# Performance work log

Measured on AMD Instinct MI355X. Metric: run time of the kernel, lower is better.

## Reference

```python
import jax, jax.numpy as jnp
import numpy as np


def _squash_global(v):
    # Faithful to torch: v.norm() with no dim -> global Frobenius norm (scalar).
    n2 = jnp.sum(v * v)
    n = jnp.sqrt(n2)
    scale = n2 / (1.0 + n2)
    return scale * v / n


def setup_inputs() -> dict:
    key = jax.random.key(0)
    k1, k2 = jax.random.split(key)
    B, R, Ci = 128, 1152, 8
    C, O = 10, 16
    x = jax.random.normal(k1, (B, R, Ci), dtype=jnp.float32)
    W = jax.random.normal(k2, (C, R, Ci, O), dtype=jnp.float32)  # routing_weights ~ randn
    return {"x": x, "W": W, "num_iterations": 3}


def reference(x, W, num_iterations):
    # prediction_vectors: [C, B, R, 1, O]
    u = jnp.einsum('bri,crio->cbro', x, W)[:, :, :, None, :]
    logits = jnp.zeros_like(u)
    v = None
    for _ in range(num_iterations):
        # batch_softmax: cat over dim0 + legacy softmax(dim=1 of 4D) == softmax over
        # the num_route_nodes axis (axis 2 here).
        c = jax.nn.softmax(logits, axis=2)
        s = jnp.sum(c * u, axis=2, keepdims=True)  # [C, B, 1, 1, O]
        v = _squash_global(s)
        logits = logits + u * v
    return v
```

## Files before the change

### kernel.cpp

```cpp
#include <hip/hip_runtime.h>
#include <math.h>

#define Bn   128
#define Rn   1152
#define CIn  8
#define Cn   10
#define On   16
#define BO   2048
#define CBO  20480
#define NSEG 18
#define XSTR 132
#define WSTR 132


template<int PASS>
__global__ __launch_bounds__(256, 2)
void pass_kernel(const float* __restrict__ X, const float* __restrict__ Wt,
                 const float* __restrict__ Sprev, const float* __restrict__ N2,
                 float* __restrict__ PT, float* __restrict__ PL)
{
    __shared__ float xs[32 * XSTR];
    __shared__ float wsh[On * WSTR];

    const int blk = blockIdx.x;
    const int c   = blk / 72;
    const int rem = blk - c * 72;
    const int bt  = rem / 18;
    const int seg = rem - bt * 18;
    const int b0  = bt * 32;
    const int rs0 = seg * 64;

    const int tid = threadIdx.x;
    const int rr  = tid & 3;
    const int og  = (tid >> 2) & 3;
    const int bq  = tid >> 4;

    float vs[2][4];
    if (PASS > 1) {
        float coef[PASS];
        #pragma unroll
        for (int t = 0; t < PASS - 1; ++t) {
            const float n2 = N2[t];
            coef[t] = n2 / ((1.0f + n2) * sqrtf(n2)) * 1.4426950408889634f;
        }
        #pragma unroll
        for (int j = 0; j < 2; ++j) {
            const int b = b0 + bq + 16 * j;
            #pragma unroll
            for (int m = 0; m < 4; ++m) {
                const int idx = c * BO + b * On + (og + 4 * m);
                float a = 0.0f;
                #pragma unroll
                for (int t = 0; t < PASS - 1; ++t)
                    a = fmaf(coef[t], Sprev[t * CBO + idx], a);
                vs[j][m] = a;
            }
        }
    }

    float tacc[2][4], lacc[2][4];
    #pragma unroll
    for (int j = 0; j < 2; ++j)
        #pragma unroll
        for (int m = 0; m < 4; ++m) { tacc[j][m] = 0.0f; lacc[j][m] = 0.0f; }

    for (int ch = 0; ch < 4; ++ch) {
        const int r0 = rs0 + ch * 16;

        {
            const float* xbase = X + (size_t)b0 * (Rn * CIn) + (size_t)r0 * CIn;
            #pragma unroll
            for (int l = tid; l < 1024; l += 256) {
                const int bl  = l >> 5;
                const int off = (l & 31) << 2;
                const float4 v = *(const float4*)(xbase + (size_t)bl * (Rn * CIn) + off);
                *(float4*)(xs + bl * XSTR + off) = v;
            }
        }
        {
            const float* wbase = Wt + (size_t)c * (Rn * CIn * On) + (size_t)r0 * (CIn * On);
            #pragma unroll
            for (int l = tid; l < 512; l += 256) {
                const int rl = l >> 5;
                const int i  = (l >> 2) & 7;
                const int o4 = (l & 3) << 2;
                const float4 v = *(const float4*)(wbase + rl * 128 + i * On + o4);
                wsh[(o4 + 0) * WSTR + rl * 8 + i] = v.x;
                wsh[(o4 + 1) * WSTR + rl * 8 + i] = v.y;
                wsh[(o4 + 2) * WSTR + rl * 8 + i] = v.z;
                wsh[(o4 + 3) * WSTR + rl * 8 + i] = v.w;
            }
        }
        __syncthreads();

        #pragma unroll
        for (int k = 0; k < 4; ++k) {
            const int r = (k << 2) | rr;
            float4 xa[2], xb[2];
            #pragma unroll
            for (int j = 0; j < 2; ++j) {
                const float* p = xs + (bq + 16 * j) * XSTR + r * 8;
                xa[j] = *(const float4*)p;
                xb[j] = *(const float4*)(p + 4);
            }
            float4 wa[4], wb[4];
            #pragma unroll
            for (int m = 0; m < 4; ++m) {
                const float* q = wsh + (og + 4 * m) * WSTR + r * 8;
                wa[m] = *(const float4*)q;
                wb[m] = *(const float4*)(q + 4);
            }
            #pragma unroll
            for (int j = 0; j < 2; ++j) {
                #pragma unroll
                for (int m = 0; m < 4; ++m) {
                    float u = xa[j].x * wa[m].x;
                    u = fmaf(xa[j].y, wa[m].y, u);
                    u = fmaf(xa[j].z, wa[m].z, u);
                    u = fmaf(xa[j].w, wa[m].w, u);
                    u = fmaf(xb[j].x, wb[m].x, u);
                    u = fmaf(xb[j].y, wb[m].y, u);
                    u = fmaf(xb[j].z, wb[m].z, u);
                    u = fmaf(xb[j].w, wb[m].w, u);
                    if (PASS == 1) {
                        tacc[j][m] += u;
                    } else {
                        const float e = exp2f(u * vs[j][m]);
                        lacc[j][m] += e;
                        tacc[j][m] = fmaf(e, u, tacc[j][m]);
                    }
                }
            }
        }
        __syncthreads();
    }

    #pragma unroll
    for (int j = 0; j < 2; ++j) {
        const int b = b0 + bq + 16 * j;
        #pragma unroll
        for (int m = 0; m < 4; ++m) {
            float tv = tacc[j][m];
            tv += __shfl_xor(tv, 1);
            tv += __shfl_xor(tv, 2);
            float lv = 0.0f;
            if (PASS > 1) {
                lv = lacc[j][m];
                lv += __shfl_xor(lv, 1);
                lv += __shfl_xor(lv, 2);
            }
            if (rr == 0) {
                const int idx = seg * CBO + c * BO + b * On + (og + 4 * m);
                PT[idx] = tv;
                if (PASS > 1) PL[idx] = lv;
            }
        }
    }
}

template<int PASS>
__global__ __launch_bounds__(256)
void combine_kernel(const float* __restrict__ PT, const float* __restrict__ PL,
                    float* __restrict__ Sout, float* __restrict__ n2out)
{
    const int i = blockIdx.x * 256 + threadIdx.x;
    float T = 0.0f, L = 0.0f;
    #pragma unroll
    for (int s = 0; s < NSEG; ++s) T += PT[s * CBO + i];
    if (PASS == 1) {
        L = (float)Rn;
    } else {
        #pragma unroll
        for (int s = 0; s < NSEG; ++s) L += PL[s * CBO + i];
    }
    const float sv = T / L;
    Sout[i] = sv;
    float sq = sv * sv;
    #pragma unroll
    for (int d = 1; d < 64; d <<= 1) sq += __shfl_xor(sq, d);
    __shared__ float red[4];
    if ((threadIdx.x & 63) == 0) red[threadIdx.x >> 6] = sq;
    __syncthreads();
    if (threadIdx.x == 0)
        atomicAdd(n2out, red[0] + red[1] + red[2] + red[3]);
}

__global__ __launch_bounds__(256)
void final_kernel(const float* __restrict__ S, const float* __restrict__ n2p,
                  float* __restrict__ out)
{
    const int i = blockIdx.x * 256 + threadIdx.x;
    const float n2 = *n2p;
    const float coef = n2 / ((1.0f + n2) * sqrtf(n2));
    out[i] = coef * S[i];
}

extern "C" void kernel_launch(void* const* d_in, const int* in_sizes, int n_in,
                              void* d_out, int out_size, void* d_ws, size_t ws_size,
                              hipStream_t stream)
{
    const float* X  = (const float*)d_in[0];
    const float* Wt = (const float*)d_in[1];
    float* ws = (float*)d_ws;
    float* N2 = ws;
    float* PT = ws + 4;
    float* PL = PT + NSEG * CBO;
    float* S  = PL + NSEG * CBO;

    hipMemsetAsync(ws, 0, 16, stream);

    pass_kernel<1><<<720, 256, 0, stream>>>(X, Wt, S, N2, PT, PL);
    combine_kernel<1><<<80, 256, 0, stream>>>(PT, PL, S + 0 * CBO, N2 + 0);
    pass_kernel<2><<<720, 256, 0, stream>>>(X, Wt, S, N2, PT, PL);
    combine_kernel<2><<<80, 256, 0, stream>>>(PT, PL, S + 1 * CBO, N2 + 1);
    pass_kernel<3><<<720, 256, 0, stream>>>(X, Wt, S, N2, PT, PL);
    combine_kernel<3><<<80, 256, 0, stream>>>(PT, PL, S + 2 * CBO, N2 + 2);
    final_kernel<<<80, 256, 0, stream>>>(S + 2 * CBO, N2 + 2, (float*)d_out);
}
```

Measured before the change: 135.1 us.

## Transpose x once and stream W through scalar loads instead of LDS tiles

Adds a one-time transpose of x into a route-major layout, so each lane (one batch element) loads its x row with coalesced float4 reads. The pass kernel no longer stages tiles in shared memory. Each wave takes a contiguous chunk of 12 routes, and W is read through wave-uniform (readfirstlane) addresses, so the hardware can serve it with scalar loads. Each thread now holds all 16 outputs for one batch element, and partial sums are reduced across the 4 waves through LDS, with fewer segments (24) left for the combine kernel. This removes the per-chunk LDS staging, barriers and transposed W stores, at the cost of an extra transpose kernel and more registers per thread.

```diff
diff --git a/kernel.cpp b/kernel.cpp
--- a/kernel.cpp
+++ b/kernel.cpp
@@ -8,34 +8,40 @@
 #define On   16
 #define BO   2048
 #define CBO  20480
-#define NSEG 18
-#define XSTR 132
-#define WSTR 132
+#define RC   12
+#define NSEG 96
+#define PSEG 24
 
+__global__ __launch_bounds__(256)
+void transpose_x(const float* __restrict__ X, float* __restrict__ XT)
+{
+    const int r = blockIdx.x;
+    const int b = threadIdx.x & 127;
+    const int g = threadIdx.x >> 7;
+    float4 v = *(const float4*)(X + (size_t)b * (Rn * CIn) + r * CIn + g * 4);
+    ((float4*)XT)[r * 256 + g * 128 + b] = v;
+}
 
 template<int PASS>
 __global__ __launch_bounds__(256, 2)
-void pass_kernel(const float* __restrict__ X, const float* __restrict__ Wt,
+void pass_kernel(const float* __restrict__ XT, const float* __restrict__ W,
                  const float* __restrict__ Sprev, const float* __restrict__ N2,
                  float* __restrict__ PT, float* __restrict__ PL)
 {
-    __shared__ float xs[32 * XSTR];
-    __shared__ float wsh[On * WSTR];
+    __shared__ float red[4][64][34];
 
-    const int blk = blockIdx.x;
-    const int c   = blk / 72;
-    const int rem = blk - c * 72;
-    const int bt  = rem / 18;
-    const int seg = rem - bt * 18;
-    const int b0  = bt * 32;
-    const int rs0 = seg * 64;
+    const int blk  = blockIdx.x;
+    const int c    = blk / 48;
+    const int rem  = blk - c * 48;
+    const int bh   = rem / 24;
+    const int segq = rem - bh * 24;
+    const int tid  = threadIdx.x;
+    const int w    = tid >> 6;
+    const int lane = tid & 63;
+    const int b    = bh * 64 + lane;
+    const int r0   = __builtin_amdgcn_readfirstlane((segq * 4 + w) * RC);
 
-    const int tid = threadIdx.x;
-    const int rr  = tid & 3;
-    const int og  = (tid >> 2) & 3;
-    const int bq  = tid >> 4;
-
-    float vs[2][4];
+    float vs[16];
     if (PASS > 1) {
         float coef[PASS];
         #pragma unroll
@@ -43,118 +49,78 @@
             const float n2 = N2[t];
             coef[t] = n2 / ((1.0f + n2) * sqrtf(n2)) * 1.4426950408889634f;
         }
+        const float* sp = Sprev + c * BO + b * On;
         #pragma unroll
-        for (int j = 0; j < 2; ++j) {
-            const int b = b0 + bq + 16 * j;
+        for (int q = 0; q < 4; ++q) {
+            float4 a = make_float4(0.f, 0.f, 0.f, 0.f);
             #pragma unroll
-            for (int m = 0; m < 4; ++m) {
-                const int idx = c * BO + b * On + (og + 4 * m);
-                float a = 0.0f;
-                #pragma unroll
-                for (int t = 0; t < PASS - 1; ++t)
-                    a = fmaf(coef[t], Sprev[t * CBO + idx], a);
-                vs[j][m] = a;
+            for (int t = 0; t < PASS - 1; ++t) {
+                const float4 s4 = *(const float4*)(sp + t * CBO + q * 4);
+                a.x = fmaf(coef[t], s4.x, a.x);
+                a.y = fmaf(coef[t], s4.y, a.y);
+                a.z = fmaf(coef[t], s4.z, a.z);
+                a.w = fmaf(coef[t], s4.w, a.w);
+            }
+            vs[q * 4 + 0] = a.x; vs[q * 4 + 1] = a.y;
+            vs[q * 4 + 2] = a.z; vs[q * 4 + 3] = a.w;
+        }
+    }
+
+    float tacc[16], lacc[16];
+    #pragma unroll
+    for (int o = 0; o < 16; ++o) { tacc[o] = 0.0f; lacc[o] = 0.0f; }
+
+    const float4* XT4 = (const float4*)XT;
+    for (int rr = 0; rr < RC; ++rr) {
+        const int r = r0 + rr;
+        const float4 xa = XT4[r * 256 + b];
+        const float4 xb = XT4[r * 256 + 128 + b];
+        const int woff = __builtin_amdgcn_readfirstlane((c * Rn + r) * 128);
+        const float* wr = W + woff;
+        #pragma unroll
+        for (int o = 0; o < 16; ++o) {
+            float u = xa.x * wr[o];
+            u = fmaf(xa.y, wr[16 + o], u);
+            u = fmaf(xa.z, wr[32 + o], u);
+            u = fmaf(xa.w, wr[48 + o], u);
+            u = fmaf(xb.x, wr[64 + o], u);
+            u = fmaf(xb.y, wr[80 + o], u);
+            u = fmaf(xb.z, wr[96 + o], u);
+            u = fmaf(xb.w, wr[112 + o], u);
+            if (PASS == 1) {
+                tacc[o] += u;
+            } else {
+                const float e = exp2f(u * vs[o]);
+                lacc[o] += e;
+                tacc[o] = fmaf(e, u, tacc[o]);
             }
         }
     }
 
-    float tacc[2][4], lacc[2][4];
     #pragma unroll
-    for (int j = 0; j < 2; ++j)
+    for (int o = 0; o < 16; ++o) {
+        red[w][lane][o]      = tacc[o];
+        red[w][lane][16 + o] = lacc[o];
+    }
+    __syncthreads();
+
+    {
+        const int bl = tid >> 2;
+        const int og = tid & 3;
+        const int bg = bh * 64 + bl;
+        float4 tv, lv;
+        float* tp = (float*)&tv;
+        float* lp = (float*)&lv;
         #pragma unroll
-        for (int m = 0; m < 4; ++m) { tacc[j][m] = 0.0f; lacc[j][m] = 0.0f; }
-
-    for (int ch = 0; ch < 4; ++ch) {
-        const int r0 = rs0 + ch * 16;
-
-        {
-            const float* xbase = X + (size_t)b0 * (Rn * CIn) + (size_t)r0 * CIn;
-            #pragma unroll
-            for (int l = tid; l < 1024; l += 256) {
-                const int bl  = l >> 5;
-                const int off = (l & 31) << 2;
-                const float4 v = *(const float4*)(xbase + (size_t)bl * (Rn * CIn) + off);
-                *(float4*)(xs + bl * XSTR + off) = v;
-            }
+        for (int q = 0; q < 4; ++q) {
+            const int o = og * 4 + q;
+            tp[q] = red[0][bl][o] + red[1][bl][o] + red[2][bl][o] + red[3][bl][o];
+            lp[q] = red[0][bl][16 + o] + red[1][bl][16 + o] +
+                    red[2][bl][16 + o] + red[3][bl][16 + o];
         }
-        {
-            const float* wbase = Wt + (size_t)c * (Rn * CIn * On) + (size_t)r0 * (CIn * On);
-            #pragma unroll
-            for (int l = tid; l < 512; l += 256) {
-                const int rl = l >> 5;
-                const int i  = (l >> 2) & 7;
-                const int o4 = (l & 3) << 2;
-                const float4 v = *(const float4*)(wbase + rl * 128 + i * On + o4);
-                wsh[(o4 + 0) * WSTR + rl * 8 + i] = v.x;
-                wsh[(o4 + 1) * WSTR + rl * 8 + i] = v.y;
-                wsh[(o4 + 2) * WSTR + rl * 8 + i] = v.z;
-                wsh[(o4 + 3) * WSTR + rl * 8 + i] = v.w;
-            }
-        }
-        __syncthreads();
-
-        #pragma unroll
-        for (int k = 0; k < 4; ++k) {
-            const int r = (k << 2) | rr;
-            float4 xa[2], xb[2];
-            #pragma unroll
-            for (int j = 0; j < 2; ++j) {
-                const float* p = xs + (bq + 16 * j) * XSTR + r * 8;
-                xa[j] = *(const float4*)p;
-                xb[j] = *(const float4*)(p + 4);
-            }
-            float4 wa[4], wb[4];
-            #pragma unroll
-            for (int m = 0; m < 4; ++m) {
-                const float* q = wsh + (og + 4 * m) * WSTR + r * 8;
-                wa[m] = *(const float4*)q;
-                wb[m] = *(const float4*)(q + 4);
-            }
-            #pragma unroll
-            for (int j = 0; j < 2; ++j) {
-                #pragma unroll
-                for (int m = 0; m < 4; ++m) {
-                    float u = xa[j].x * wa[m].x;
-                    u = fmaf(xa[j].y, wa[m].y, u);
-                    u = fmaf(xa[j].z, wa[m].z, u);
-                    u = fmaf(xa[j].w, wa[m].w, u);
-                    u = fmaf(xb[j].x, wb[m].x, u);
-                    u = fmaf(xb[j].y, wb[m].y, u);
-                    u = fmaf(xb[j].z, wb[m].z, u);
-                    u = fmaf(xb[j].w, wb[m].w, u);
-                    if (PASS == 1) {
-                        tacc[j][m] += u;
-                    } else {
-                        const float e = exp2f(u * vs[j][m]);
-                        lacc[j][m] += e;
-                        tacc[j][m] = fmaf(e, u, tacc[j][m]);
-                    }
-                }
-            }
-        }
-        __syncthreads();
-    }
-
-    #pragma unroll
-    for (int j = 0; j < 2; ++j) {
-        const int b = b0 + bq + 16 * j;
-        #pragma unroll
-        for (int m = 0; m < 4; ++m) {
-            float tv = tacc[j][m];
-            tv += __shfl_xor(tv, 1);
-            tv += __shfl_xor(tv, 2);
-            float lv = 0.0f;
-            if (PASS > 1) {
-                lv = lacc[j][m];
-                lv += __shfl_xor(lv, 1);
-                lv += __shfl_xor(lv, 2);
-            }
-            if (rr == 0) {
-                const int idx = seg * CBO + c * BO + b * On + (og + 4 * m);
-                PT[idx] = tv;
-                if (PASS > 1) PL[idx] = lv;
-            }
-        }
+        const int idx = segq * CBO + c * BO + bg * On + og * 4;
+        *(float4*)(PT + idx) = tv;
+        if (PASS > 1) *(float4*)(PL + idx) = lv;
     }
 }
 
@@ -166,12 +132,12 @@
     const int i = blockIdx.x * 256 + threadIdx.x;
     float T = 0.0f, L = 0.0f;
     #pragma unroll
-    for (int s = 0; s < NSEG; ++s) T += PT[s * CBO + i];
+    for (int s = 0; s < PSEG; ++s) T += PT[s * CBO + i];
     if (PASS == 1) {
         L = (float)Rn;
     } else {
         #pragma unroll
-        for (int s = 0; s < NSEG; ++s) L += PL[s * CBO + i];
+        for (int s = 0; s < PSEG; ++s) L += PL[s * CBO + i];
     }
     const float sv = T / L;
     Sout[i] = sv;
@@ -199,21 +165,23 @@
                               void* d_out, int out_size, void* d_ws, size_t ws_size,
                               hipStream_t stream)
 {
-    const float* X  = (const float*)d_in[0];
-    const float* Wt = (const float*)d_in[1];
+    const float* X = (const float*)d_in[0];
+    const float* W = (const float*)d_in[1];
     float* ws = (float*)d_ws;
-    float* N2 = ws;
-    float* PT = ws + 4;
-    float* PL = PT + NSEG * CBO;
-    float* S  = PL + NSEG * CBO;
+    float* XT = ws;
+    float* N2 = XT + Rn * Bn * CIn;
+    float* PT = N2 + 4;
+    float* PL = PT + PSEG * CBO;
+    float* S  = PL + PSEG * CBO;
 
-    hipMemsetAsync(ws, 0, 16, stream);
+    hipMemsetAsync(N2, 0, 16, stream);
 
-    pass_kernel<1><<<720, 256, 0, stream>>>(X, Wt, S, N2, PT, PL);
+    transpose_x<<<Rn, 256, 0, stream>>>(X, XT);
+    pass_kernel<1><<<480, 256, 0, stream>>>(XT, W, S, N2, PT, PL);
     combine_kernel<1><<<80, 256, 0, stream>>>(PT, PL, S + 0 * CBO, N2 + 0);
-    pass_kernel<2><<<720, 256, 0, stream>>>(X, Wt, S, N2, PT, PL);
+    pass_kernel<2><<<480, 256, 0, stream>>>(XT, W, S, N2, PT, PL);
     combine_kernel<2><<<80, 256, 0, stream>>>(PT, PL, S + 1 * CBO, N2 + 1);
-    pass_kernel<3><<<720, 256, 0, stream>>>(X, Wt, S, N2, PT, PL);
+    pass_kernel<3><<<480, 256, 0, stream>>>(XT, W, S, N2, PT, PL);
     combine_kernel<3><<<80, 256, 0, stream>>>(PT, PL, S + 2 * CBO, N2 + 2);
     final_kernel<<<80, 256, 0, stream>>>(S + 2 * CBO, N2 + 2, (float*)d_out);
 }
```

Measured after the change: 124.5 us. 1.08x faster.
